# Performance work log

Measured on AMD Instinct MI355X. Metric: run time of the kernel, lower is better.

Reference implementation:

```python
import jax, jax.numpy as jnp
import numpy as np

B, T1 = 256, 64            # batch, number of transition steps (T-1)
S, A = 128, 32             # state_size, action_size
BEL, HID, EMB = 1024, 1024, 1024
MIN_STD = 0.1


def _lin(key, out_dim, in_dim):
    k1, k2 = jax.random.split(key)
    s = 1.0 / np.sqrt(in_dim)
    W = jax.random.uniform(k1, (out_dim, in_dim), jnp.float32, -s, s)
    b = jax.random.uniform(k2, (out_dim,), jnp.float32, -s, s)
    return W, b


def setup_inputs() -> dict:
    key = jax.random.key(0)
    ks = jax.random.split(key, 16)
    W_sa, b_sa = _lin(ks[0], BEL, S + A)
    # GRUCell weights (torch layout: [3H, in]/[3H, H], gate order r,z,n)
    sg = 1.0 / np.sqrt(BEL)
    W_ih = jax.random.uniform(ks[1], (3 * BEL, BEL), jnp.float32, -sg, sg)
    W_hh = jax.random.uniform(ks[2], (3 * BEL, BEL), jnp.float32, -sg, sg)
    b_ih = jax.random.uniform(ks[3], (3 * BEL,), jnp.float32, -sg, sg)
    b_hh = jax.random.uniform(ks[4], (3 * BEL,), jnp.float32, -sg, sg)
    W_bp, b_bp = _lin(ks[5], HID, BEL)
    W_sp, b_sp = _lin(ks[6], 2 * S, HID)
    W_bq, b_bq = _lin(ks[7], HID, BEL + EMB)
    W_sq, b_sq = _lin(ks[8], 2 * S, HID)
    return {
        "prev_state": jax.random.normal(ks[9], (B, S), jnp.float32),
        "actions": jax.random.normal(ks[10], (T1, B, A), jnp.float32),
        "prev_belief": jax.random.normal(ks[11], (B, BEL), jnp.float32),
        "observations": jax.random.normal(ks[12], (T1, B, EMB), jnp.float32),
        "nonterminals": jnp.ones((T1, B, 1), jnp.float32),
        "prior_noise": jax.random.normal(ks[13], (T1, B, S), jnp.float32),
        "post_noise": jax.random.normal(ks[14], (T1, B, S), jnp.float32),
        "W_sa": W_sa, "b_sa": b_sa,
        "W_ih": W_ih, "W_hh": W_hh, "b_ih": b_ih, "b_hh": b_hh,
        "W_bp": W_bp, "b_bp": b_bp, "W_sp": W_sp, "b_sp": b_sp,
        "W_bq": W_bq, "b_bq": b_bq, "W_sq": W_sq, "b_sq": b_sq,
    }


def reference(prev_state, actions, prev_belief, observations, nonterminals,
              prior_noise, post_noise,
              W_sa, b_sa, W_ih, W_hh, b_ih, b_hh,
              W_bp, b_bp, W_sp, b_sp, W_bq, b_bq, W_sq, b_sq):
    # nonterminals[t-1] is applied for t>=1; t==0 uses no mask -> prepend ones
    nt_eff = jnp.concatenate([jnp.ones_like(nonterminals[:1]), nonterminals[:-1]], axis=0)

    def step(carry, inp):
        belief, state = carry
        a, obs, nt, pn, qn = inp
        s = state * nt
        x = jax.nn.relu(jnp.concatenate([s, a], axis=-1) @ W_sa.T + b_sa)
        h = belief * nt
        # torch GRUCell: gates r,z,n
        gi = x @ W_ih.T + b_ih
        gh = h @ W_hh.T + b_hh
        ir, iz, in_ = jnp.split(gi, 3, axis=-1)
        hr, hz, hn = jnp.split(gh, 3, axis=-1)
        r = jax.nn.sigmoid(ir + hr)
        z = jax.nn.sigmoid(iz + hz)
        n = jnp.tanh(in_ + r * hn)
        nb = (1.0 - z) * n + z * h  # new belief [B, BEL]
        # prior head
        hp = jax.nn.relu(nb @ W_bp.T + b_bp)
        pm, psd_raw = jnp.split(hp @ W_sp.T + b_sp, 2, axis=-1)
        psd = jax.nn.softplus(psd_raw) + MIN_STD
        ps = pm + psd * pn
        # posterior head
        hq = jax.nn.relu(jnp.concatenate([nb, obs], axis=-1) @ W_bq.T + b_bq)
        qm, qsd_raw = jnp.split(hq @ W_sq.T + b_sq, 2, axis=-1)
        qsd = jax.nn.softplus(qsd_raw) + MIN_STD
        qs = qm + qsd * qn
        return (nb, qs), (nb, ps, pm, psd, qs, qm, qsd)

    _, outs = jax.lax.scan(step, (prev_belief, prev_state),
                           (actions, observations, nt_eff, prior_noise, post_noise))
    beliefs, prior_states, prior_means, prior_stds, post_states, post_means, post_stds = outs
    return beliefs, prior_states, prior_means, prior_stds, post_states, post_means, post_stds
```

## Files before the change

kernel.cpp:

```cpp
#include <hip/hip_runtime.h>
#include <math.h>

constexpr int NB = 256, NT = 64, DS = 128, DA = 32, DB = 1024, DH = 1024, DE = 1024;
constexpr float MIN_STD = 0.1f;

constexpr size_t OUT_PS  = (size_t)NT * NB * DB;
constexpr size_t OUT_PM  = OUT_PS  + (size_t)NT * NB * DS;
constexpr size_t OUT_PSD = OUT_PM  + (size_t)NT * NB * DS;
constexpr size_t OUT_QS  = OUT_PSD + (size_t)NT * NB * DS;
constexpr size_t OUT_QM  = OUT_QS  + (size_t)NT * NB * DS;
constexpr size_t OUT_QSD = OUT_QM  + (size_t)NT * NB * DS;

typedef __attribute__((ext_vector_type(8))) short bf8_t;
typedef __attribute__((ext_vector_type(4))) float f4_t;
#define MFMA16(a, b, c) __builtin_amdgcn_mfma_f32_16x16x32_bf16((a), (b), (c), 0, 0, 0)
#define SWZ8(ch, row) ((ch & ~7) | ((ch & 7) ^ ((row) & 7)))

__device__ __forceinline__ short f2bf(float f) {
    union { float f; unsigned u; } v; v.f = f;
    unsigned r = v.u + 0x7FFF + ((v.u >> 16) & 1);
    return (short)(r >> 16);
}
__device__ __forceinline__ float bf2f(unsigned short h) {
    union { unsigned u; float f; } v; v.u = ((unsigned)h) << 16; return v.f;
}
__device__ __forceinline__ unsigned pack2(float a, float b) {
    return ((unsigned)(unsigned short)f2bf(a)) | (((unsigned)(unsigned short)f2bf(b)) << 16);
}
__device__ __forceinline__ float sigm(float x) { return 1.0f / (1.0f + __expf(-x)); }

__global__ __launch_bounds__(256) void k_cvt_all(
    const float* __restrict__ Wih, const float* __restrict__ Whh,
    const float* __restrict__ Wbp, const float* __restrict__ Wbq,
    const float* __restrict__ Wsp, const float* __restrict__ Wsq,
    const float* __restrict__ Wsa,
    short* dWbp, short* dWbq, short* dWsp, short* dWsq,
    short* dWsqsw, short* dWsasw, short* dWbqnb, short* dWihsw, short* dWhhsw)
{
    int i = blockIdx.x * 256 + threadIdx.x;
    if (i >= 1429504) return;
    if (i >= 512000 && i < 643072) {
        int il = i - 512000;
        int c = il >> 7, kc = il & 127;
        const float4* s4 = (const float4*)Wbq;
        float4 a = s4[(size_t)c * 512 + kc * 2], b = s4[(size_t)c * 512 + kc * 2 + 1];
        bf8_t v;
        v[0]=f2bf(a.x); v[1]=f2bf(a.y); v[2]=f2bf(a.z); v[3]=f2bf(a.w);
        v[4]=f2bf(b.x); v[5]=f2bf(b.y); v[6]=f2bf(b.z); v[7]=f2bf(b.w);
        ((bf8_t*)dWbqnb)[((size_t)((c >> 4) * 128 + kc)) * 16 + (c & 15)] = v;
        return;
    }
    const float* src; short* dst; int lo; bool sw = false; int swNCH = 0;
    if      (i <  131072) { src = Wbp; dst = dWbp; lo = 0; }
    else if (i <  393216) { src = Wbq; dst = dWbq; lo = 131072; }
    else if (i <  425984) { src = Wsp; dst = dWsp; lo = 393216; }
    else if (i <  458752) { src = Wsq; dst = dWsq; lo = 425984; }
    else if (i <  491520) { src = Wsq; dst = dWsqsw; lo = 458752; sw = true; swNCH = 128; }
    else if (i <  512000) { src = Wsa; dst = dWsasw; lo = 491520; sw = true; swNCH = 20; }
    else if (i < 1036288) { src = Wih; dst = dWihsw; lo = 643072;  sw = true; swNCH = 128; }
    else                  { src = Whh; dst = dWhhsw; lo = 1036288; sw = true; swNCH = 128; }
    int il = i - lo;
    const float4* s4 = (const float4*)src;
    float4 a = s4[il * 2], b = s4[il * 2 + 1];
    bf8_t v;
    v[0]=f2bf(a.x); v[1]=f2bf(a.y); v[2]=f2bf(a.z); v[3]=f2bf(a.w);
    v[4]=f2bf(b.x); v[5]=f2bf(b.y); v[6]=f2bf(b.z); v[7]=f2bf(b.w);
    if (!sw) ((bf8_t*)dst)[il] = v;
    else {
        int row = il / swNCH, ch = il % swNCH;
        ((bf8_t*)dst)[((row >> 4) * swNCH + ch) * 16 + (row & 15)] = v;
    }
}

__global__ __launch_bounds__(256) void kobs(
    const float* __restrict__ obsA, const short* __restrict__ Wbq_bf,
    const float* __restrict__ b_bq, short* __restrict__ dst)
{
    __shared__ __align__(16) char smem[16384];
    const int tx = threadIdx.x;
    const int wv = tx >> 6, lane = tx & 63;
    const int b0 = blockIdx.x * 64, j0 = blockIdx.y * 64;
    const int wm = wv & 1, wn = wv >> 1;
    const bf8_t* Wq8 = (const bf8_t*)Wbq_bf;
    bf8_t* sA = (bf8_t*)smem;
    bf8_t* sB = sA + 512;
    f4_t acc[2][2];
    acc[0][0] = (f4_t)0.0f; acc[0][1] = (f4_t)0.0f;
    acc[1][0] = (f4_t)0.0f; acc[1][1] = (f4_t)0.0f;

    for (int kt = 0; kt < DE; kt += 64) {
        #pragma unroll
        for (int i = 0; i < 2; ++i) {
            int c = tx + i * 256;
            int row = c >> 3, ch = c & 7;
            const float4* p4 = (const float4*)(obsA + (size_t)(b0 + row) * DE + kt + ch * 8);
            float4 f0 = p4[0], f1 = p4[1];
            bf8_t v;
            v[0]=f2bf(f0.x); v[1]=f2bf(f0.y); v[2]=f2bf(f0.z); v[3]=f2bf(f0.w);
            v[4]=f2bf(f1.x); v[5]=f2bf(f1.y); v[6]=f2bf(f1.z); v[7]=f2bf(f1.w);
            sA[row * 8 + (ch ^ (row & 7))] = v;
            sB[row * 8 + (ch ^ (row & 7))] = Wq8[(size_t)(j0 + row) * 256 + 128 + (kt >> 3) + ch];
        }
        __syncthreads();
        #pragma unroll
        for (int ks = 0; ks < 2; ++ks) {
            int ch = ks * 4 + (lane >> 4);
            bf8_t a[2], b[2];
            #pragma unroll
            for (int mi = 0; mi < 2; ++mi) {
                int row = wm * 32 + mi * 16 + (lane & 15);
                a[mi] = sA[row * 8 + (ch ^ (row & 7))];
            }
            #pragma unroll
            for (int ni = 0; ni < 2; ++ni) {
                int row = wn * 32 + ni * 16 + (lane & 15);
                b[ni] = sB[row * 8 + (ch ^ (row & 7))];
            }
            #pragma unroll
            for (int mi = 0; mi < 2; ++mi)
                #pragma unroll
                for (int ni = 0; ni < 2; ++ni)
                    acc[mi][ni] = MFMA16(a[mi], b[ni], acc[mi][ni]);
        }
        __syncthreads();
    }
    float* ebuf = (float*)smem;
    #pragma unroll
    for (int mi = 0; mi < 2; ++mi)
        #pragma unroll
        for (int ni = 0; ni < 2; ++ni)
            #pragma unroll
            for (int r = 0; r < 4; ++r) {
                int row = wm * 32 + mi * 16 + (lane >> 4) * 4 + r;
                int col = wn * 32 + ni * 16 + (lane & 15);
                ebuf[row * 64 + col] = acc[mi][ni][r] + b_bq[j0 + col];
            }
    __syncthreads();
    {
        int bl = tx >> 2, p = tx & 3;
        float* src = ebuf + bl * 64 + p * 16;
        short* d = dst + (size_t)(b0 + bl) * DB + j0 + p * 16;
        #pragma unroll
        for (int q = 0; q < 4; ++q) {
            uint2 u; u.x = pack2(src[q*4], src[q*4+1]); u.y = pack2(src[q*4+2], src[q*4+3]);
            *(uint2*)(d + q * 4) = u;
        }
    }
}

__global__ __launch_bounds__(1024) void kstep(
    int t,
    const float* __restrict__ prev_state, const float* __restrict__ actions_t,
    const float* __restrict__ nonterm, const float* __restrict__ post_noise,
    const short* __restrict__ part_in, const short* __restrict__ obs_pre_tm1,
    const short* __restrict__ Wsq_sw, const float* __restrict__ b_sq,
    const short* __restrict__ Wsa_sw, const float* __restrict__ b_sa,
    const short* __restrict__ Wih_sw, const short* __restrict__ Whh_sw,
    const float* __restrict__ b_ih, const float* __restrict__ b_hh,
    const short* __restrict__ Wbqnb_sw,
    const float* __restrict__ belp,
    float* __restrict__ bel_out, short* __restrict__ part_out,
    float* __restrict__ o_qm, float* __restrict__ o_qsd, float* __restrict__ o_qs)
{
    __shared__ __align__(16) char smem[120064];
    short* R1s = (short*)smem;
    bf8_t* R18 = (bf8_t*)smem;
    float* qex = (float*)smem;
    bf8_t* hf8 = (bf8_t*)(smem + 32768);
    bf8_t* sP  = (bf8_t*)(smem + 32768);
    short* sPs = (short*)(smem + 32768);
    short* saS = (short*)(smem + 65536);
    bf8_t* sa8 = (bf8_t*)(smem + 65536);
    float* exg = (float*)(smem + 70912);

    const int tx = threadIdx.x, bid = blockIdx.x;
    const int wv = tx >> 6, lane = tx & 63;
    const int ar = lane & 15, kq = lane >> 4;
    const int bgrp = bid >> 4, low = bid & 15;
    const int jt = ((low & 7) << 1) | (low >> 3);
    const int b0 = bgrp * 16, j0 = jt * 64;
    const float* ntp = (t > 0) ? nonterm + (size_t)(t - 1) * NB : nullptr;

    #pragma unroll
    for (int i = 0; i < 2; ++i) {
        int c = tx + i * 1024;
        int row = c >> 7, ch = c & 127;
        int b = b0 + row;
        const float4* p4 = (const float4*)(belp + (size_t)b * DB + ch * 8);
        float4 f0 = p4[0], f1 = p4[1];
        float ntv = ntp ? ntp[b] : 1.0f;
        bf8_t v;
        v[0]=f2bf(f0.x*ntv); v[1]=f2bf(f0.y*ntv); v[2]=f2bf(f0.z*ntv); v[3]=f2bf(f0.w*ntv);
        v[4]=f2bf(f1.x*ntv); v[5]=f2bf(f1.y*ntv); v[6]=f2bf(f1.z*ntv); v[7]=f2bf(f1.w*ntv);
        hf8[row * 128 + SWZ8(ch, row)] = v;
    }

    if (t > 0) {
        #pragma unroll
        for (int i = 0; i < 2; ++i) {
            int c = tx + i * 1024;
            int row = c >> 7, ch = c & 127;
            const bf8_t o8 = ((const bf8_t*)obs_pre_tm1)[(size_t)(b0 + row) * 128 + ch];
            float s[8];
            #pragma unroll
            for (int e = 0; e < 8; ++e) s[e] = bf2f((unsigned short)o8[e]);
            #pragma unroll
            for (int p = 0; p < 16; ++p) {
                const bf8_t v = ((const bf8_t*)part_in)[((size_t)p * NB + b0 + row) * 128 + ch];
                #pragma unroll
                for (int e = 0; e < 8; ++e) s[e] += bf2f((unsigned short)v[e]);
            }
            bf8_t r;
            #pragma unroll
            for (int e = 0; e < 8; ++e) r[e] = f2bf(fmaxf(s[e], 0.0f));
            R18[row * 128 + SWZ8(ch, row)] = r;
        }
        __syncthreads();
        {
            f4_t qa[4];
            #pragma unroll
            for (int i = 0; i < 4; ++i) qa[i] = (f4_t)0.0f;
            for (int ks = 0; ks < 32; ks += 4) {
                #pragma unroll
                for (int u = 0; u < 4; ++u) {
                    int ch = (ks + u) * 4 + kq;
                    bf8_t a = R18[ar * 128 + SWZ8(ch, ar)];
                    bf8_t bfr = *(const bf8_t*)(Wsq_sw +
                        ((size_t)(wv * 128 + ch)) * 128 + ar * 8);
                    qa[u] = MFMA16(a, bfr, qa[u]);
                }
            }
            f4_t qs_ = (qa[0] + qa[1]) + (qa[2] + qa[3]);
            __syncthreads();
            #pragma unroll
            for (int r = 0; r < 4; ++r)
                qex[(kq * 4 + r) * 257 + wv * 16 + ar] = qs_[r];
        }
        __syncthreads();
        #pragma unroll
        for (int i = 0; i < 2; ++i) {
            int e = tx + i * 1024;
            int row = e >> 7, col = e & 127;
            int b = b0 + row;
            float m  = qex[row * 257 + col] + b_sq[col];
            float sr = qex[row * 257 + 128 + col] + b_sq[128 + col];
            float sd = log1pf(__expf(-fabsf(sr))) + fmaxf(sr, 0.0f) + MIN_STD;
            float n_ = post_noise[((size_t)(t - 1) * NB + b) * DS + col];
            float qs = fmaf(sd, n_, m);
            if (jt == 0) {
                size_t off = ((size_t)(t - 1) * NB + b) * DS + col;
                o_qm[off] = m; o_qsd[off] = sd; o_qs[off] = qs;
            }
            saS[row * 168 + col] = f2bf(qs * ntp[b]);
        }
    } else {
        #pragma unroll
        for (int i = 0; i < 2; ++i) {
            int e = tx + i * 1024;
            int row = e >> 7, col = e & 127;
            saS[row * 168 + col] = f2bf(prev_state[(size_t)(b0 + row) * DS + col]);
        }
    }
    if (tx < 512) {
        int row = tx >> 5, ac = tx & 31;
        saS[row * 168 + 128 + ac] = f2bf(actions_t[(size_t)(b0 + row) * DA + ac]);
    }
    __syncthreads();

    {
        f4_t xacc[4];
        #pragma unroll
        for (int i = 0; i < 4; ++i) xacc[i] = (f4_t)0.0f;
        #pragma unroll
        for (int ks = 0; ks < 5; ++ks) {
            int ch = ks * 4 + kq;
            bf8_t a = sa8[ar * 21 + ch];
            #pragma unroll
            for (int i = 0; i < 4; ++i) {
                int tile = wv * 4 + i;
                bf8_t bfr = *(const bf8_t*)(Wsa_sw +
                    ((size_t)(tile * 20 + ch)) * 128 + ar * 8);
                xacc[i] = MFMA16(a, bfr, xacc[i]);
            }
        }
        #pragma unroll
        for (int i = 0; i < 4; ++i) {
            int col = (wv * 4 + i) * 16 + ar;
            float bj = b_sa[col];
            int chunk = col >> 3, el = col & 7;
            #pragma unroll
            for (int r = 0; r < 4; ++r) {
                int row = kq * 4 + r;
                R1s[row * 1024 + SWZ8(chunk, row) * 8 + el] =
                    f2bf(fmaxf(xacc[i][r] + bj, 0.0f));
            }
        }
    }
    __syncthreads();

    {
        const int kh = wv >> 3, wg = (wv >> 2) & 1, wn = wv & 3;
        f4_t acc[3];
        acc[0] = (f4_t)0.0f; acc[1] = (f4_t)0.0f; acc[2] = (f4_t)0.0f;
        const bf8_t* Asrc = wg ? hf8 : R18;
        const short* Wsw = wg ? Whh_sw : Wih_sw;
        #pragma unroll 4
        for (int k16 = 0; k16 < 16; ++k16) {
            int chunk = kh * 64 + k16 * 4 + kq;
            bf8_t a = Asrc[ar * 128 + SWZ8(chunk, ar)];
            #pragma unroll
            for (int g = 0; g < 3; ++g) {
                bf8_t bfr = *(const bf8_t*)(Wsw +
                    (((size_t)(g * 64 + jt * 4 + wn) * 128 + chunk) * 16 + ar) * 8);
                acc[g] = MFMA16(a, bfr, acc[g]);
            }
        }
        #pragma unroll
        for (int g = 0; g < 3; ++g)
            #pragma unroll
            for (int r = 0; r < 4; ++r)
                exg[((wv * 3 + g) * 16 + (kq * 4 + r)) * 16 + ar] = acc[g][r];
    }
    __syncthreads();
    {
        const int row = tx >> 6;
        const int col = tx & 63;
        const int wn2 = col >> 4, cl = col & 15;
        const int j = j0 + col;
        float gi[3], gh[3];
        #pragma unroll
        for (int g = 0; g < 3; ++g) {
            gi[g] = exg[(((0  + wn2) * 3 + g) * 16 + row) * 16 + cl]
                  + exg[(((8  + wn2) * 3 + g) * 16 + row) * 16 + cl];
            gh[g] = exg[(((4  + wn2) * 3 + g) * 16 + row) * 16 + cl]
                  + exg[(((12 + wn2) * 3 + g) * 16 + row) * 16 + cl];
        }
        const int b = b0 + row;
        const float ntv = ntp ? ntp[b] : 1.0f;
        const float h = belp[(size_t)b * DB + j] * ntv;
        const float rr = sigm(gi[0] + b_ih[j] + gh[0] + b_hh[j]);
        const float zz = sigm(gi[1] + b_ih[DB + j] + gh[1] + b_hh[DB + j]);
        const float nn = tanhf(gi[2] + b_ih[2 * DB + j] + rr * (gh[2] + b_hh[2 * DB + j]));
        const float nbv = (1.0f - zz) * nn + zz * h;
        bel_out[(size_t)b * DB + j] = nbv;
        sPs[row * 64 + ((((col >> 3) ^ (row & 7)) << 3) | (col & 7))] = f2bf(nbv);
    }
    __syncthreads();
    {
        f4_t pacc[4];
        #pragma unroll
        for (int i = 0; i < 4; ++i) pacc[i] = (f4_t)0.0f;
        #pragma unroll
        for (int ks = 0; ks < 2; ++ks) {
            int ch = ks * 4 + kq;
            bf8_t a = sP[ar * 8 + (ch ^ (ar & 7))];
            #pragma unroll
            for (int i = 0; i < 4; ++i) {
                int tile = wv * 4 + i;
                bf8_t bfr = *(const bf8_t*)(Wbqnb_sw +
                    (((size_t)tile * 128 + jt * 8 + ch) * 16 + ar) * 8);
                pacc[i] = MFMA16(a, bfr, pacc[i]);
            }
        }
        #pragma unroll
        for (int i = 0; i < 4; ++i) {
            int c = (wv * 4 + i) * 16 + ar;
            #pragma unroll
            for (int r = 0; r < 4; ++r)
                part_out[((size_t)jt * NB + b0 + kq * 4 + r) * DB + c] = f2bf(pacc[i][r]);
        }
    }
}

__global__ __launch_bounds__(256) void khq63(
    const short* __restrict__ partials, const short* __restrict__ obs_pre,
    short* __restrict__ hqb)
{
    const int row = blockIdx.x;
    const int c = threadIdx.x * 4;
    const ushort4 o = *(const ushort4*)(obs_pre + (size_t)row * DB + c);
    float s0 = bf2f(o.x), s1 = bf2f(o.y), s2 = bf2f(o.z), s3 = bf2f(o.w);
    for (int p = 0; p < 16; ++p) {
        const ushort4 v = *(const ushort4*)(partials + ((size_t)p * NB + row) * DB + c);
        s0 += bf2f(v.x); s1 += bf2f(v.y); s2 += bf2f(v.z); s3 += bf2f(v.w);
    }
    uint2 u;
    u.x = pack2(fmaxf(s0, 0.0f), fmaxf(s1, 0.0f));
    u.y = pack2(fmaxf(s2, 0.0f), fmaxf(s3, 0.0f));
    *(uint2*)(hqb + (size_t)row * DB + c) = u;
}

__global__ __launch_bounds__(256) void kout(
    const short* __restrict__ A_, const short* __restrict__ W_,
    const float* __restrict__ bias, const float* __restrict__ noise,
    float* __restrict__ om, float* __restrict__ osd, float* __restrict__ os)
{
    __shared__ __align__(16) char smem[12288];
    const int tx = threadIdx.x;
    const int wv = tx >> 6, lane = tx & 63;
    const int b0 = blockIdx.x * 64, i0 = blockIdx.y * 16;
    const int wm = wv & 1, wn = wv >> 1;
    const bf8_t* A8 = (const bf8_t*)A_;
    const bf8_t* W8 = (const bf8_t*)W_;
    bf8_t* sA = (bf8_t*)smem;
    bf8_t* sB = sA + 512;
    f4_t acc[2];
    acc[0] = (f4_t)0.0f; acc[1] = (f4_t)0.0f;

    for (int kt = 0; kt < DH; kt += 64) {
        #pragma unroll
        for (int i = 0; i < 2; ++i) {
            int c = tx + i * 256;
            int row = c >> 3, ch = c & 7;
            sA[row * 8 + (ch ^ (row & 7))] = A8[(size_t)(b0 + row) * 128 + (kt >> 3) + ch];
        }
        {
            int row = tx >> 3, ch = tx & 7;
            int wr = (row < 16) ? (i0 + row) : (128 + i0 + (row - 16));
            sB[row * 8 + (ch ^ (row & 7))] = W8[(size_t)wr * 128 + (kt >> 3) + ch];
        }
        __syncthreads();
        #pragma unroll
        for (int ks = 0; ks < 2; ++ks) {
            int ch = ks * 4 + (lane >> 4);
            bf8_t a[2], b;
            #pragma unroll
            for (int mi = 0; mi < 2; ++mi) {
                int row = wm * 32 + mi * 16 + (lane & 15);
                a[mi] = sA[row * 8 + (ch ^ (row & 7))];
            }
            {
                int row = wn * 16 + (lane & 15);
                b = sB[row * 8 + (ch ^ (row & 7))];
            }
            acc[0] = MFMA16(a[0], b, acc[0]);
            acc[1] = MFMA16(a[1], b, acc[1]);
        }
        __syncthreads();
    }
    float* ebuf = (float*)smem;
    #pragma unroll
    for (int mi = 0; mi < 2; ++mi)
        #pragma unroll
        for (int r = 0; r < 4; ++r) {
            int row = wm * 32 + mi * 16 + (lane >> 4) * 4 + r;
            int col = wn * 16 + (lane & 15);
            ebuf[row * 32 + col] = acc[mi][r];
        }
    __syncthreads();
    {
        int bl = tx >> 2, p = tx & 3;
        int b = b0 + bl;
        float4 vm, vs, vx;
        #pragma unroll
        for (int k = 0; k < 4; ++k) {
            int i = p * 4 + k;
            float m_ = ebuf[bl * 32 + i] + bias[i0 + i];
            float sraw = ebuf[bl * 32 + 16 + i] + bias[128 + i0 + i];
            float sd = log1pf(__expf(-fabsf(sraw))) + fmaxf(sraw, 0.0f) + MIN_STD;
            float n_ = noise[(size_t)b * DS + i0 + i];
            ((float*)&vm)[k] = m_;
            ((float*)&vs)[k] = sd;
            ((float*)&vx)[k] = fmaf(sd, n_, m_);
        }
        size_t off = (size_t)b * DS + i0 + p * 4;
        *(float4*)(om + off)  = vm;
        *(float4*)(osd + off) = vs;
        *(float4*)(os + off)  = vx;
    }
}

__global__ __launch_bounds__(256) void khp(
    const float* __restrict__ belA, const short* __restrict__ Wbp_bf,
    const float* __restrict__ b_bp, short* __restrict__ hp_bf)
{
    __shared__ __align__(16) char smem[16384];
    const int tx = threadIdx.x;
    const int wv = tx >> 6, lane = tx & 63;
    const int b0 = blockIdx.x * 64, j0 = blockIdx.y * 64;
    const int wm = wv & 1, wn = wv >> 1;
    const bf8_t* Wp8 = (const bf8_t*)Wbp_bf;
    bf8_t* sA = (bf8_t*)smem;
    bf8_t* sB = sA + 512;
    f4_t acc[2][2];
    acc[0][0] = (f4_t)0.0f; acc[0][1] = (f4_t)0.0f;
    acc[1][0] = (f4_t)0.0f; acc[1][1] = (f4_t)0.0f;

    for (int kt = 0; kt < DB; kt += 64) {
        #pragma unroll
        for (int i = 0; i < 2; ++i) {
            int c = tx + i * 256;
            int row = c >> 3, ch = c & 7;
            const float4* p4 = (const float4*)(belA + (size_t)(b0 + row) * DB + kt + ch * 8);
            float4 f0 = p4[0], f1 = p4[1];
            bf8_t v;
            v[0]=f2bf(f0.x); v[1]=f2bf(f0.y); v[2]=f2bf(f0.z); v[3]=f2bf(f0.w);
            v[4]=f2bf(f1.x); v[5]=f2bf(f1.y); v[6]=f2bf(f1.z); v[7]=f2bf(f1.w);
            sA[row * 8 + (ch ^ (row & 7))] = v;
            sB[row * 8 + (ch ^ (row & 7))] = Wp8[(size_t)(j0 + row) * 128 + (kt >> 3) + ch];
        }
        __syncthreads();
        #pragma unroll
        for (int ks = 0; ks < 2; ++ks) {
            int ch = ks * 4 + (lane >> 4);
            bf8_t a[2], b[2];
            #pragma unroll
            for (int mi = 0; mi < 2; ++mi) {
                int row = wm * 32 + mi * 16 + (lane & 15);
                a[mi] = sA[row * 8 + (ch ^ (row & 7))];
            }
            #pragma unroll
            for (int ni = 0; ni < 2; ++ni) {
                int row = wn * 32 + ni * 16 + (lane & 15);
                b[ni] = sB[row * 8 + (ch ^ (row & 7))];
            }
            #pragma unroll
            for (int mi = 0; mi < 2; ++mi)
                #pragma unroll
                for (int ni = 0; ni < 2; ++ni)
                    acc[mi][ni] = MFMA16(a[mi], b[ni], acc[mi][ni]);
        }
        __syncthreads();
    }
    float* ebuf = (float*)smem;
    #pragma unroll
    for (int mi = 0; mi < 2; ++mi)
        #pragma unroll
        for (int ni = 0; ni < 2; ++ni)
            #pragma unroll
            for (int r = 0; r < 4; ++r) {
                int row = wm * 32 + mi * 16 + (lane >> 4) * 4 + r;
                int col = wn * 32 + ni * 16 + (lane & 15);
                ebuf[row * 64 + col] = fmaxf(acc[mi][ni][r] + b_bp[j0 + col], 0.0f);
            }
    __syncthreads();
    {
        int bl = tx >> 2, p = tx & 3;
        float* src = ebuf + bl * 64 + p * 16;
        short* dst = hp_bf + (size_t)(b0 + bl) * DH + j0 + p * 16;
        #pragma unroll
        for (int q = 0; q < 4; ++q) {
            uint2 u; u.x = pack2(src[q*4], src[q*4+1]); u.y = pack2(src[q*4+2], src[q*4+3]);
            *(uint2*)(dst + q * 4) = u;
        }
    }
}

extern "C" void kernel_launch(void* const* d_in, const int* in_sizes, int n_in,
                              void* d_out, int out_size, void* d_ws, size_t ws_size,
                              hipStream_t stream)
{
    const float* prev_state   = (const float*)d_in[0];
    const float* actions      = (const float*)d_in[1];
    const float* prev_belief  = (const float*)d_in[2];
    const float* observations = (const float*)d_in[3];
    const float* nonterm      = (const float*)d_in[4];
    const float* prior_noise  = (const float*)d_in[5];
    const float* post_noise   = (const float*)d_in[6];
    const float* W_sa = (const float*)d_in[7];
    const float* b_sa = (const float*)d_in[8];
    const float* W_ih = (const float*)d_in[9];
    const float* W_hh = (const float*)d_in[10];
    const float* b_ih = (const float*)d_in[11];
    const float* b_hh = (const float*)d_in[12];
    const float* W_bp = (const float*)d_in[13];
    const float* b_bp = (const float*)d_in[14];
    const float* W_sp = (const float*)d_in[15];
    const float* b_sp = (const float*)d_in[16];
    const float* W_bq = (const float*)d_in[17];
    const float* b_bq = (const float*)d_in[18];
    const float* W_sq = (const float*)d_in[19];
    const float* b_sq = (const float*)d_in[20];

    float* out     = (float*)d_out;
    float* beliefs = out;
    float* o_ps  = out + OUT_PS;
    float* o_pm  = out + OUT_PM;
    float* o_psd = out + OUT_PSD;
    float* o_qs  = out + OUT_QS;
    float* o_qm  = out + OUT_QM;
    float* o_qsd = out + OUT_QSD;

    short* w = (short*)d_ws;
    short* Wbp_bf   = w;
    short* Wbq_bf   = Wbp_bf   + (size_t)1048576;
    short* Wsp_bf   = Wbq_bf   + (size_t)2097152;
    short* Wsq_bf   = Wsp_bf   + (size_t)262144;
    short* Wsq_sw   = Wsq_bf   + (size_t)262144;
    short* Wsa_sw   = Wsq_sw   + (size_t)262144;
    short* Wbqnb_sw = Wsa_sw   + (size_t)163840;
    short* Wih_sw   = Wbqnb_sw + (size_t)1048576;
    short* Whh_sw   = Wih_sw   + (size_t)3145728;
    short* obs_all  = Whh_sw   + (size_t)3145728;
    short* partials = obs_all  + (size_t)16777216;
    short* hqb      = partials + (size_t)8388608;
    short* hp_bf    = partials;
    const size_t PART = (size_t)16 * NB * DB;

    k_cvt_all<<<5584, 256, 0, stream>>>(
        W_ih, W_hh, W_bp, W_bq, W_sp, W_sq, W_sa,
        Wbp_bf, Wbq_bf, Wsp_bf, Wsq_bf, Wsq_sw, Wsa_sw, Wbqnb_sw, Wih_sw, Whh_sw);

    kobs<<<dim3(256, 16), 256, 0, stream>>>(observations, Wbq_bf, b_bq, obs_all);

    for (int t = 0; t < NT; ++t) {
        const float* belp = (t == 0) ? prev_belief : beliefs + (size_t)(t - 1) * NB * DB;
        kstep<<<256, 1024, 0, stream>>>(
            t, prev_state, actions + (size_t)t * NB * DA,
            nonterm, post_noise,
            partials + ((t & 1) ^ 1) * PART,
            obs_all + (size_t)(t > 0 ? t - 1 : 0) * NB * DB,
            Wsq_sw, b_sq, Wsa_sw, b_sa,
            Wih_sw, Whh_sw, b_ih, b_hh, Wbqnb_sw,
            belp, beliefs + (size_t)t * NB * DB,
            partials + (t & 1) * PART,
            o_qm, o_qsd, o_qs);
    }

    khq63<<<256, 256, 0, stream>>>(
        partials + ((NT - 1) & 1) * PART, obs_all + (size_t)(NT - 1) * NB * DB, hqb);
    kout<<<dim3(4, 8), 256, 0, stream>>>(
        hqb, Wsq_bf, b_sq, post_noise + (size_t)(NT - 1) * NB * DS,
        o_qm + (size_t)(NT - 1) * NB * DS, o_qsd + (size_t)(NT - 1) * NB * DS,
        o_qs + (size_t)(NT - 1) * NB * DS);

    for (int c = 0; c < 2; ++c) {
        const size_t r0 = (size_t)c * 8192;
        khp<<<dim3(128, 16), 256, 0, stream>>>(
            beliefs + r0 * DB, Wbp_bf, b_bp, hp_bf);
        kout<<<dim3(128, 8), 256, 0, stream>>>(
            hp_bf, Wsp_bf, b_sp, prior_noise + r0 * DS,
            o_pm + r0 * DS, o_psd + r0 * DS, o_ps + r0 * DS);
    }
}
```

Before: 2.599 ms.

## Overlap hidden-state GRU matmul with posterior head in step kernel; restructure obs GEMM

```diff
diff --git a/kernel.cpp b/kernel.cpp
--- a/kernel.cpp
+++ b/kernel.cpp
@@ -35,10 +35,22 @@
     const float* __restrict__ Wsp, const float* __restrict__ Wsq,
     const float* __restrict__ Wsa,
     short* dWbp, short* dWbq, short* dWsp, short* dWsq,
-    short* dWsqsw, short* dWsasw, short* dWbqnb, short* dWihsw, short* dWhhsw)
+    short* dWsqsw, short* dWsasw, short* dWbqnb, short* dWihsw, short* dWhhsw,
+    short* dWbqob)
 {
     int i = blockIdx.x * 256 + threadIdx.x;
-    if (i >= 1429504) return;
+    if (i >= 1560576) return;
+    if (i >= 1429504) {
+        int il = i - 1429504;
+        int c = il >> 7, kc = il & 127;
+        const float4* s4 = (const float4*)Wbq;
+        float4 a = s4[(size_t)c * 512 + 256 + kc * 2], b = s4[(size_t)c * 512 + 256 + kc * 2 + 1];
+        bf8_t v;
+        v[0]=f2bf(a.x); v[1]=f2bf(a.y); v[2]=f2bf(a.z); v[3]=f2bf(a.w);
+        v[4]=f2bf(b.x); v[5]=f2bf(b.y); v[6]=f2bf(b.z); v[7]=f2bf(b.w);
+        ((bf8_t*)dWbqob)[((size_t)((c >> 4) * 128 + kc)) * 16 + (c & 15)] = v;
+        return;
+    }
     if (i >= 512000 && i < 643072) {
         int il = i - 512000;
         int c = il >> 7, kc = il & 127;
@@ -72,79 +84,67 @@
     }
 }
 
-__global__ __launch_bounds__(256) void kobs(
-    const float* __restrict__ obsA, const short* __restrict__ Wbq_bf,
+__global__ __launch_bounds__(512) void kobs(
+    const float* __restrict__ obsA, const short* __restrict__ Wbqob_sw,
     const float* __restrict__ b_bq, short* __restrict__ dst)
 {
-    __shared__ __align__(16) char smem[16384];
+    __shared__ __align__(16) char smem[147456];
+    bf8_t* A = (bf8_t*)smem;
+    float* ebuf = (float*)(smem + 131072);
+
     const int tx = threadIdx.x;
     const int wv = tx >> 6, lane = tx & 63;
-    const int b0 = blockIdx.x * 64, j0 = blockIdx.y * 64;
-    const int wm = wv & 1, wn = wv >> 1;
-    const bf8_t* Wq8 = (const bf8_t*)Wbq_bf;
-    bf8_t* sA = (bf8_t*)smem;
-    bf8_t* sB = sA + 512;
-    f4_t acc[2][2];
-    acc[0][0] = (f4_t)0.0f; acc[0][1] = (f4_t)0.0f;
-    acc[1][0] = (f4_t)0.0f; acc[1][1] = (f4_t)0.0f;
-
-    for (int kt = 0; kt < DE; kt += 64) {
-        #pragma unroll
-        for (int i = 0; i < 2; ++i) {
-            int c = tx + i * 256;
-            int row = c >> 3, ch = c & 7;
-            const float4* p4 = (const float4*)(obsA + (size_t)(b0 + row) * DE + kt + ch * 8);
-            float4 f0 = p4[0], f1 = p4[1];
-            bf8_t v;
-            v[0]=f2bf(f0.x); v[1]=f2bf(f0.y); v[2]=f2bf(f0.z); v[3]=f2bf(f0.w);
-            v[4]=f2bf(f1.x); v[5]=f2bf(f1.y); v[6]=f2bf(f1.z); v[7]=f2bf(f1.w);
-            sA[row * 8 + (ch ^ (row & 7))] = v;
-            sB[row * 8 + (ch ^ (row & 7))] = Wq8[(size_t)(j0 + row) * 256 + 128 + (kt >> 3) + ch];
-        }
+    const int ar = lane & 15, kq = lane >> 4;
+    const int b0 = blockIdx.x * 64;
+    const int ct = wv & 3, rt0 = (wv >> 2) * 2;
+
+    #pragma unroll
+    for (int i = 0; i < 16; ++i) {
+        int c = tx + i * 512;
+        int row = c >> 7, ch = c & 127;
+        const float4* p4 = (const float4*)(obsA + (size_t)(b0 + row) * DE + ch * 8);
+        float4 f0 = p4[0], f1 = p4[1];
+        bf8_t v;
+        v[0]=f2bf(f0.x); v[1]=f2bf(f0.y); v[2]=f2bf(f0.z); v[3]=f2bf(f0.w);
+        v[4]=f2bf(f1.x); v[5]=f2bf(f1.y); v[6]=f2bf(f1.z); v[7]=f2bf(f1.w);
+        A[row * 128 + SWZ8(ch, row)] = v;
+    }
+    __syncthreads();
+
+    for (int jt = 0; jt < 16; ++jt) {
+        f4_t acc[2];
+        acc[0] = (f4_t)0.0f; acc[1] = (f4_t)0.0f;
+        for (int ks = 0; ks < 32; ++ks) {
+            int ch = ks * 4 + kq;
+            bf8_t bfr = *(const bf8_t*)(Wbqob_sw +
+                (((size_t)(jt * 4 + ct) * 128 + ch) * 16 + ar) * 8);
+            #pragma unroll
+            for (int r = 0; r < 2; ++r) {
+                int row = (rt0 + r) * 16 + ar;
+                bf8_t a = A[row * 128 + SWZ8(ch, row)];
+                acc[r] = MFMA16(a, bfr, acc[r]);
+            }
+        }
+        #pragma unroll
+        for (int r = 0; r < 2; ++r)
+            #pragma unroll
+            for (int q = 0; q < 4; ++q)
+                ebuf[((rt0 + r) * 16 + kq * 4 + q) * 64 + ct * 16 + ar] = acc[r][q];
         __syncthreads();
-        #pragma unroll
-        for (int ks = 0; ks < 2; ++ks) {
-            int ch = ks * 4 + (lane >> 4);
-            bf8_t a[2], b[2];
-            #pragma unroll
-            for (int mi = 0; mi < 2; ++mi) {
-                int row = wm * 32 + mi * 16 + (lane & 15);
-                a[mi] = sA[row * 8 + (ch ^ (row & 7))];
-            }
-            #pragma unroll
-            for (int ni = 0; ni < 2; ++ni) {
-                int row = wn * 32 + ni * 16 + (lane & 15);
-                b[ni] = sB[row * 8 + (ch ^ (row & 7))];
-            }
-            #pragma unroll
-            for (int mi = 0; mi < 2; ++mi)
-                #pragma unroll
-                for (int ni = 0; ni < 2; ++ni)
-                    acc[mi][ni] = MFMA16(a[mi], b[ni], acc[mi][ni]);
+        {
+            int row = tx >> 3, p = tx & 7;
+            float* src = ebuf + row * 64 + p * 8;
+            int colb = jt * 64 + p * 8;
+            uint2 u;
+            u.x = pack2(src[0] + b_bq[colb],     src[1] + b_bq[colb + 1]);
+            u.y = pack2(src[2] + b_bq[colb + 2], src[3] + b_bq[colb + 3]);
+            uint2 u2;
+            u2.x = pack2(src[4] + b_bq[colb + 4], src[5] + b_bq[colb + 5]);
+            u2.y = pack2(src[6] + b_bq[colb + 6], src[7] + b_bq[colb + 7]);
+            uint4 w; w.x = u.x; w.y = u.y; w.z = u2.x; w.w = u2.y;
+            *(uint4*)(dst + (size_t)(b0 + row) * DB + colb) = w;
         }
         __syncthreads();
-    }
-    float* ebuf = (float*)smem;
-    #pragma unroll
-    for (int mi = 0; mi < 2; ++mi)
-        #pragma unroll
-        for (int ni = 0; ni < 2; ++ni)
-            #pragma unroll
-            for (int r = 0; r < 4; ++r) {
-                int row = wm * 32 + mi * 16 + (lane >> 4) * 4 + r;
-                int col = wn * 32 + ni * 16 + (lane & 15);
-                ebuf[row * 64 + col] = acc[mi][ni][r] + b_bq[j0 + col];
-            }
-    __syncthreads();
-    {
-        int bl = tx >> 2, p = tx & 3;
-        float* src = ebuf + bl * 64 + p * 16;
-        short* d = dst + (size_t)(b0 + bl) * DB + j0 + p * 16;
-        #pragma unroll
-        for (int q = 0; q < 4; ++q) {
-            uint2 u; u.x = pack2(src[q*4], src[q*4+1]); u.y = pack2(src[q*4+2], src[q*4+3]);
-            *(uint2*)(d + q * 4) = u;
-        }
     }
 }
 
@@ -162,16 +162,16 @@
     float* __restrict__ bel_out, short* __restrict__ part_out,
     float* __restrict__ o_qm, float* __restrict__ o_qsd, float* __restrict__ o_qs)
 {
-    __shared__ __align__(16) char smem[120064];
+    __shared__ __align__(16) char smem[136960];
     short* R1s = (short*)smem;
     bf8_t* R18 = (bf8_t*)smem;
-    float* qex = (float*)smem;
     bf8_t* hf8 = (bf8_t*)(smem + 32768);
     bf8_t* sP  = (bf8_t*)(smem + 32768);
     short* sPs = (short*)(smem + 32768);
     short* saS = (short*)(smem + 65536);
     bf8_t* sa8 = (bf8_t*)(smem + 65536);
     float* exg = (float*)(smem + 70912);
+    float* qex = (float*)(smem + 120064);
 
     const int tx = threadIdx.x, bid = blockIdx.x;
     const int wv = tx >> 6, lane = tx & 63;
@@ -180,6 +180,27 @@
     const int jt = ((low & 7) << 1) | (low >> 3);
     const int b0 = bgrp * 16, j0 = jt * 64;
     const float* ntp = (t > 0) ? nonterm + (size_t)(t - 1) * NB : nullptr;
+    const bool xside = (wv < 8);
+    const int wx = wv & 7;
+
+    f4_t hacc[3];
+    hacc[0] = (f4_t)0.0f; hacc[1] = (f4_t)0.0f; hacc[2] = (f4_t)0.0f;
+    const int hkh = wx >> 2, hwn = wx & 3;
+
+#define GH_PART(K0)                                                            \
+    {                                                                          \
+        _Pragma("unroll")                                                      \
+        for (int k16 = (K0); k16 < (K0) + 4; ++k16) {                          \
+            int chunk = hkh * 64 + k16 * 4 + kq;                               \
+            bf8_t a = hf8[ar * 128 + SWZ8(chunk, ar)];                         \
+            _Pragma("unroll")                                                  \
+            for (int g = 0; g < 3; ++g) {                                      \
+                bf8_t bfr = *(const bf8_t*)(Whh_sw +                           \
+                    (((size_t)(g * 64 + jt * 4 + hwn) * 128 + chunk) * 16 + ar) * 8); \
+                hacc[g] = MFMA16(a, bfr, hacc[g]);                             \
+            }                                                                  \
+        }                                                                      \
+    }
 
     #pragma unroll
     for (int i = 0; i < 2; ++i) {
@@ -194,98 +215,118 @@
         v[4]=f2bf(f1.x*ntv); v[5]=f2bf(f1.y*ntv); v[6]=f2bf(f1.z*ntv); v[7]=f2bf(f1.w*ntv);
         hf8[row * 128 + SWZ8(ch, row)] = v;
     }
-
-    if (t > 0) {
-        #pragma unroll
-        for (int i = 0; i < 2; ++i) {
-            int c = tx + i * 1024;
-            int row = c >> 7, ch = c & 127;
-            const bf8_t o8 = ((const bf8_t*)obs_pre_tm1)[(size_t)(b0 + row) * 128 + ch];
-            float s[8];
-            #pragma unroll
-            for (int e = 0; e < 8; ++e) s[e] = bf2f((unsigned short)o8[e]);
-            #pragma unroll
-            for (int p = 0; p < 16; ++p) {
-                const bf8_t v = ((const bf8_t*)part_in)[((size_t)p * NB + b0 + row) * 128 + ch];
+    __syncthreads();
+
+    if (xside) {
+        if (t > 0) {
+            #pragma unroll
+            for (int i = 0; i < 4; ++i) {
+                int c = tx + i * 512;
+                int row = c >> 7, ch = c & 127;
+                const bf8_t o8 = ((const bf8_t*)obs_pre_tm1)[(size_t)(b0 + row) * 128 + ch];
+                float s[8];
                 #pragma unroll
-                for (int e = 0; e < 8; ++e) s[e] += bf2f((unsigned short)v[e]);
-            }
-            bf8_t r;
-            #pragma unroll
-            for (int e = 0; e < 8; ++e) r[e] = f2bf(fmaxf(s[e], 0.0f));
-            R18[row * 128 + SWZ8(ch, row)] = r;
-        }
-        __syncthreads();
+                for (int e = 0; e < 8; ++e) s[e] = bf2f((unsigned short)o8[e]);
+                #pragma unroll
+                for (int p = 0; p < 16; ++p) {
+                    const bf8_t v = ((const bf8_t*)part_in)[((size_t)p * NB + b0 + row) * 128 + ch];
+                    #pragma unroll
+                    for (int e = 0; e < 8; ++e) s[e] += bf2f((unsigned short)v[e]);
+                }
+                bf8_t r;
+                #pragma unroll
+                for (int e = 0; e < 8; ++e) r[e] = f2bf(fmaxf(s[e], 0.0f));
+                R18[row * 128 + SWZ8(ch, row)] = r;
+            }
+        } else {
+            #pragma unroll
+            for (int i = 0; i < 4; ++i) {
+                int c = tx + i * 512;
+                int row = c >> 7, col = c & 127;
+                saS[row * 168 + col] = f2bf(prev_state[(size_t)(b0 + row) * DS + col]);
+            }
+        }
         {
-            f4_t qa[4];
-            #pragma unroll
-            for (int i = 0; i < 4; ++i) qa[i] = (f4_t)0.0f;
-            for (int ks = 0; ks < 32; ks += 4) {
+            int row = tx >> 5, ac = tx & 31;
+            saS[row * 168 + 128 + ac] = f2bf(actions_t[(size_t)(b0 + row) * DA + ac]);
+        }
+    } else {
+        GH_PART(0)
+    }
+    __syncthreads();
+
+    if (xside) {
+        if (t > 0) {
+            #pragma unroll
+            for (int tt = 0; tt < 2; ++tt) {
+                int tile = wx + tt * 8;
+                f4_t qa[4];
                 #pragma unroll
-                for (int u = 0; u < 4; ++u) {
-                    int ch = (ks + u) * 4 + kq;
-                    bf8_t a = R18[ar * 128 + SWZ8(ch, ar)];
-                    bf8_t bfr = *(const bf8_t*)(Wsq_sw +
-                        ((size_t)(wv * 128 + ch)) * 128 + ar * 8);
-                    qa[u] = MFMA16(a, bfr, qa[u]);
+                for (int i = 0; i < 4; ++i) qa[i] = (f4_t)0.0f;
+                for (int ks = 0; ks < 32; ks += 4) {
+                    #pragma unroll
+                    for (int u = 0; u < 4; ++u) {
+                        int ch = (ks + u) * 4 + kq;
+                        bf8_t a = R18[ar * 128 + SWZ8(ch, ar)];
+                        bf8_t bfr = *(const bf8_t*)(Wsq_sw +
+                            ((size_t)(tile * 128 + ch)) * 128 + ar * 8);
+                        qa[u] = MFMA16(a, bfr, qa[u]);
+                    }
                 }
-            }
-            f4_t qs_ = (qa[0] + qa[1]) + (qa[2] + qa[3]);
-            __syncthreads();
-            #pragma unroll
-            for (int r = 0; r < 4; ++r)
-                qex[(kq * 4 + r) * 257 + wv * 16 + ar] = qs_[r];
-        }
-        __syncthreads();
-        #pragma unroll
-        for (int i = 0; i < 2; ++i) {
-            int e = tx + i * 1024;
-            int row = e >> 7, col = e & 127;
-            int b = b0 + row;
-            float m  = qex[row * 257 + col] + b_sq[col];
-            float sr = qex[row * 257 + 128 + col] + b_sq[128 + col];
-            float sd = log1pf(__expf(-fabsf(sr))) + fmaxf(sr, 0.0f) + MIN_STD;
-            float n_ = post_noise[((size_t)(t - 1) * NB + b) * DS + col];
-            float qs = fmaf(sd, n_, m);
-            if (jt == 0) {
-                size_t off = ((size_t)(t - 1) * NB + b) * DS + col;
-                o_qm[off] = m; o_qsd[off] = sd; o_qs[off] = qs;
-            }
-            saS[row * 168 + col] = f2bf(qs * ntp[b]);
+                f4_t qs_ = (qa[0] + qa[1]) + (qa[2] + qa[3]);
+                #pragma unroll
+                for (int r = 0; r < 4; ++r)
+                    qex[(kq * 4 + r) * 257 + tile * 16 + ar] = qs_[r];
+            }
         }
     } else {
-        #pragma unroll
-        for (int i = 0; i < 2; ++i) {
-            int e = tx + i * 1024;
-            int row = e >> 7, col = e & 127;
-            saS[row * 168 + col] = f2bf(prev_state[(size_t)(b0 + row) * DS + col]);
-        }
-    }
-    if (tx < 512) {
-        int row = tx >> 5, ac = tx & 31;
-        saS[row * 168 + 128 + ac] = f2bf(actions_t[(size_t)(b0 + row) * DA + ac]);
-    }
-    __syncthreads();
-
-    {
-        f4_t xacc[4];
-        #pragma unroll
-        for (int i = 0; i < 4; ++i) xacc[i] = (f4_t)0.0f;
+        GH_PART(4)
+    }
+    __syncthreads();
+
+    if (xside) {
+        if (t > 0) {
+            #pragma unroll
+            for (int i = 0; i < 4; ++i) {
+                int e = tx + i * 512;
+                int row = e >> 7, col = e & 127;
+                int b = b0 + row;
+                float m  = qex[row * 257 + col] + b_sq[col];
+                float sr = qex[row * 257 + 128 + col] + b_sq[128 + col];
+                float sd = log1pf(__expf(-fabsf(sr))) + fmaxf(sr, 0.0f) + MIN_STD;
+                float n_ = post_noise[((size_t)(t - 1) * NB + b) * DS + col];
+                float qs = fmaf(sd, n_, m);
+                if (jt == 0) {
+                    size_t off = ((size_t)(t - 1) * NB + b) * DS + col;
+                    o_qm[off] = m; o_qsd[off] = sd; o_qs[off] = qs;
+                }
+                saS[row * 168 + col] = f2bf(qs * ntp[b]);
+            }
+        }
+    } else {
+        GH_PART(8)
+    }
+    __syncthreads();
+
+    if (xside) {
+        f4_t xacc[8];
+        #pragma unroll
+        for (int i = 0; i < 8; ++i) xacc[i] = (f4_t)0.0f;
         #pragma unroll
         for (int ks = 0; ks < 5; ++ks) {
             int ch = ks * 4 + kq;
             bf8_t a = sa8[ar * 21 + ch];
             #pragma unroll
-            for (int i = 0; i < 4; ++i) {
-                int tile = wv * 4 + i;
+            for (int i = 0; i < 8; ++i) {
+                int tile = wx * 8 + i;
                 bf8_t bfr = *(const bf8_t*)(Wsa_sw +
                     ((size_t)(tile * 20 + ch)) * 128 + ar * 8);
                 xacc[i] = MFMA16(a, bfr, xacc[i]);
             }
         }
         #pragma unroll
-        for (int i = 0; i < 4; ++i) {
-            int col = (wv * 4 + i) * 16 + ar;
+        for (int i = 0; i < 8; ++i) {
+            int col = (wx * 8 + i) * 16 + ar;
             float bj = b_sa[col];
             int chunk = col >> 3, el = col & 7;
             #pragma unroll
@@ -295,33 +336,41 @@
                     f2bf(fmaxf(xacc[i][r] + bj, 0.0f));
             }
         }
-    }
-    __syncthreads();
-
-    {
-        const int kh = wv >> 3, wg = (wv >> 2) & 1, wn = wv & 3;
+    } else {
+        GH_PART(12)
+        const int slot = hkh * 8 + 4 + hwn;
+        #pragma unroll
+        for (int g = 0; g < 3; ++g)
+            #pragma unroll
+            for (int r = 0; r < 4; ++r)
+                exg[((slot * 3 + g) * 16 + (kq * 4 + r)) * 16 + ar] = hacc[g][r];
+    }
+    __syncthreads();
+
+    if (xside) {
+        const int ikh = wx >> 2, iwn = wx & 3;
         f4_t acc[3];
         acc[0] = (f4_t)0.0f; acc[1] = (f4_t)0.0f; acc[2] = (f4_t)0.0f;
-        const bf8_t* Asrc = wg ? hf8 : R18;
-        const short* Wsw = wg ? Whh_sw : Wih_sw;
         #pragma unroll 4
         for (int k16 = 0; k16 < 16; ++k16) {
-            int chunk = kh * 64 + k16 * 4 + kq;
-            bf8_t a = Asrc[ar * 128 + SWZ8(chunk, ar)];
+            int chunk = ikh * 64 + k16 * 4 + kq;
+            bf8_t a = R18[ar * 128 + SWZ8(chunk, ar)];
             #pragma unroll
             for (int g = 0; g < 3; ++g) {
-                bf8_t bfr = *(const bf8_t*)(Wsw +
-                    (((size_t)(g * 64 + jt * 4 + wn) * 128 + chunk) * 16 + ar) * 8);
+                bf8_t bfr = *(const bf8_t*)(Wih_sw +
+                    (((size_t)(g * 64 + jt * 4 + iwn) * 128 + chunk) * 16 + ar) * 8);
                 acc[g] = MFMA16(a, bfr, acc[g]);
             }
         }
+        const int slot = ikh * 8 + iwn;
         #pragma unroll
         for (int g = 0; g < 3; ++g)
             #pragma unroll
             for (int r = 0; r < 4; ++r)
-                exg[((wv * 3 + g) * 16 + (kq * 4 + r)) * 16 + ar] = acc[g][r];
-    }
-    __syncthreads();
+                exg[((slot * 3 + g) * 16 + (kq * 4 + r)) * 16 + ar] = acc[g][r];
+    }
+    __syncthreads();
+
     {
         const int row = tx >> 6;
         const int col = tx & 63;
@@ -346,6 +395,7 @@
         sPs[row * 64 + ((((col >> 3) ^ (row & 7)) << 3) | (col & 7))] = f2bf(nbv);
     }
     __syncthreads();
+
     {
         f4_t pacc[4];
         #pragma unroll
@@ -370,6 +420,7 @@
                 part_out[((size_t)jt * NB + b0 + kq * 4 + r) * DB + c] = f2bf(pacc[i][r]);
         }
     }
+#undef GH_PART
 }
 
 __global__ __launch_bounds__(256) void khq63(
@@ -589,7 +640,8 @@
     short* Wsq_sw   = Wsq_bf   + (size_t)262144;
     short* Wsa_sw   = Wsq_sw   + (size_t)262144;
     short* Wbqnb_sw = Wsa_sw   + (size_t)163840;
-    short* Wih_sw   = Wbqnb_sw + (size_t)1048576;
+    short* Wbqob_sw = Wbqnb_sw + (size_t)1048576;
+    short* Wih_sw   = Wbqob_sw + (size_t)1048576;
     short* Whh_sw   = Wih_sw   + (size_t)3145728;
     short* obs_all  = Whh_sw   + (size_t)3145728;
     short* partials = obs_all  + (size_t)16777216;
@@ -597,11 +649,12 @@
     short* hp_bf    = partials;
     const size_t PART = (size_t)16 * NB * DB;
 
-    k_cvt_all<<<5584, 256, 0, stream>>>(
+    k_cvt_all<<<6096, 256, 0, stream>>>(
         W_ih, W_hh, W_bp, W_bq, W_sp, W_sq, W_sa,
-        Wbp_bf, Wbq_bf, Wsp_bf, Wsq_bf, Wsq_sw, Wsa_sw, Wbqnb_sw, Wih_sw, Whh_sw);
-
-    kobs<<<dim3(256, 16), 256, 0, stream>>>(observations, Wbq_bf, b_bq, obs_all);
+        Wbp_bf, Wbq_bf, Wsp_bf, Wsq_bf, Wsq_sw, Wsa_sw, Wbqnb_sw, Wih_sw, Whh_sw,
+        Wbqob_sw);
+
+    kobs<<<256, 512, 0, stream>>>(observations, Wbqob_sw, b_bq, obs_all);
 
     for (int t = 0; t < NT; ++t) {
         const float* belp = (t == 0) ? prev_belief : beliefs + (size_t)(t - 1) * NB * DB;
```

Measured after the change: 3.122 ms. +20.1%, slower.
